# Performance work log

Measured on AMD Instinct MI355X. Metric: run time of the kernel, lower is better.

## Reference

```python
import jax, jax.numpy as jnp
import numpy as np

B, NV, L, NKG = 8, 100, 128, 923
NT = NV + 1 + NKG  # 1024 total nodes
DV, DK, DH, H, NLAYERS, VOCAB = 2048, 300, 1024, 8, 3, 50265
DHD = DH // H


def _ln(x, g, b, eps=1e-5):
    m = x.mean(-1, keepdims=True)
    v = x.var(-1, keepdims=True)
    return (x - m) / jnp.sqrt(v + eps) * g + b


def _gat_layer(x, mask, W, bb, a_src, a_dst, ln_g, ln_b):
    # x: [B,N,D], mask: [B,N,N] bool
    Bn, N, D = x.shape
    h = (x @ W + bb).reshape(Bn, N, H, DHD)
    s = jnp.einsum('bnhd,hd->bnh', h, a_src)  # source term
    t = jnp.einsum('bnhd,hd->bnh', h, a_dst)  # target term
    e = jax.nn.leaky_relu(s[:, :, None, :] + t[:, None, :, :], 0.2)  # [B,N,N,H]
    e = jnp.where(mask[..., None], e, -1e9)
    a = jax.nn.softmax(e, axis=2)  # over neighbors j
    out = jnp.einsum('bijh,bjhd->bihd', a, h).reshape(Bn, N, D)
    return _ln(x + out, ln_g, ln_b)


def setup_inputs() -> dict:
    key = jax.random.key(0)
    ks = jax.random.split(key, 24)
    s = 0.02
    inp = {
        'visual_features': jax.random.normal(ks[0], (B, NV, DV), jnp.float32),
        'question_input_ids': jax.random.randint(ks[1], (B, L), 0, VOCAB, jnp.int64) if False else jax.random.randint(ks[1], (B, L), 0, VOCAB).astype(jnp.int32),
        'question_attention_mask': jnp.ones((B, L), jnp.int32),
        'graph_node_features': jax.random.normal(ks[2], (B, NKG, DK), jnp.float32),
        'graph_adj': jax.random.randint(ks[3], (B, NT, NT), 0, 2).astype(jnp.int32),
        'graph_node_types': jax.random.randint(ks[4], (B, NT), 0, 3).astype(jnp.int32),
        # params
        'vis_W': jax.random.normal(ks[5], (DV, DH), jnp.float32) * s,
        'vis_b': jnp.zeros((DH,), jnp.float32),
        'vis_ln_g': jnp.ones((DH,), jnp.float32),
        'vis_ln_b': jnp.zeros((DH,), jnp.float32),
        'tok_emb': jax.random.normal(ks[6], (VOCAB, DH), jnp.float32) * s,
        'q_W': jax.random.normal(ks[7], (DH, DH), jnp.float32) * s,
        'q_b': jnp.zeros((DH,), jnp.float32),
        'q_ln_g': jnp.ones((DH,), jnp.float32),
        'q_ln_b': jnp.zeros((DH,), jnp.float32),
        'kg_W': jax.random.normal(ks[8], (DK, DH), jnp.float32) * s,
        'kg_b': jnp.zeros((DH,), jnp.float32),
        'kg_ln_g': jnp.ones((DH,), jnp.float32),
        'kg_ln_b': jnp.zeros((DH,), jnp.float32),
        'type_emb': jax.random.normal(ks[9], (3, DH), jnp.float32) * s,
        'gat_W': jax.random.normal(ks[10], (NLAYERS, DH, DH), jnp.float32) * s,
        'gat_b': jnp.zeros((NLAYERS, DH), jnp.float32),
        'a_src': jax.random.normal(ks[11], (NLAYERS, H, DHD), jnp.float32) * s,
        'a_dst': jax.random.normal(ks[12], (NLAYERS, H, DHD), jnp.float32) * s,
        'gat_ln_g': jnp.ones((NLAYERS, DH), jnp.float32),
        'gat_ln_b': jnp.zeros((NLAYERS, DH), jnp.float32),
        'readout_W': jax.random.normal(ks[13], (DH, 1), jnp.float32) * s,
        'readout_b': jnp.zeros((1,), jnp.float32),
        'cs_W1': jax.random.normal(ks[14], (DH, DH), jnp.float32) * s,
        'cs_b1': jnp.zeros((DH,), jnp.float32),
        'cs_W2': jax.random.normal(ks[15], (DH, 1), jnp.float32) * s,
        'cs_b2': jnp.zeros((1,), jnp.float32),
    }
    return inp


def reference(visual_features, question_input_ids, question_attention_mask,
              graph_node_features, graph_adj, graph_node_types,
              vis_W, vis_b, vis_ln_g, vis_ln_b,
              tok_emb, q_W, q_b, q_ln_g, q_ln_b,
              kg_W, kg_b, kg_ln_g, kg_ln_b,
              type_emb, gat_W, gat_b, a_src, a_dst, gat_ln_g, gat_ln_b,
              readout_W, readout_b, cs_W1, cs_b1, cs_W2, cs_b2):
    # 1. visual projection
    vis = _ln(visual_features @ vis_W + vis_b, vis_ln_g, vis_ln_b)  # [B,NV,DH]
    # 2. text encoder (embedding + masked mean-pool + proj + LN)
    te = tok_emb[question_input_ids]  # [B,L,DH]
    m = question_attention_mask.astype(te.dtype)[..., None]
    pooled = (te * m).sum(1) / jnp.maximum(m.sum(1), 1.0)
    q = _ln(pooled @ q_W + q_b, q_ln_g, q_ln_b)[:, None, :]  # [B,1,DH]
    # 3. KG projection
    kg = _ln(graph_node_features @ kg_W + kg_b, kg_ln_g, kg_ln_b)
    # 4-5. concat + node-type embeddings
    x = jnp.concatenate([vis, q, kg], axis=1) + type_emb[graph_node_types]
    # 6. dense GAT stack
    mask = graph_adj > 0
    for l in range(NLAYERS):
        x = _gat_layer(x, mask, gat_W[l], gat_b[l], a_src[l], a_dst[l],
                       gat_ln_g[l], gat_ln_b[l])
    # 7. attention-pooled readout
    w = jax.nn.softmax((x @ readout_W + readout_b).squeeze(-1), axis=-1)
    g = (x * w[..., None]).sum(1)  # [B,DH]
    # 8. candidate scorer
    logits = jax.nn.gelu(g @ cs_W1 + cs_b1) @ cs_W2 + cs_b2  # [B,1]
    return logits
```

## Files before the change

kernel.cpp:

```cpp
#include <hip/hip_runtime.h>
#include <math.h>

#define NB 8
#define NV 100
#define LQ 128
#define NKG 923
#define NT 1024
#define DV 2048
#define DK 300
#define DH 1024
#define NH 8
#define DHD 128
#define NLAYERS 3

typedef __attribute__((ext_vector_type(8))) short short8;
typedef __attribute__((ext_vector_type(4))) float f32x4;

__device__ __forceinline__ short f2bf(float f) {
    unsigned u = __float_as_uint(f);
    u += 0x7fff + ((u >> 16) & 1);
    return (short)(u >> 16);
}
__device__ __forceinline__ float bf2f(short s) {
    unsigned u = ((unsigned)(unsigned short)s) << 16;
    return __uint_as_float(u);
}
__device__ __forceinline__ unsigned pack2(float a, float b) {
    return (unsigned)(unsigned short)f2bf(a) | ((unsigned)(unsigned short)f2bf(b) << 16);
}

#if __has_builtin(__builtin_amdgcn_global_load_lds)
#define HAVE_GLL 1
__device__ __forceinline__ void gll16(const void* g, void* l) {
    __builtin_amdgcn_global_load_lds(
        (const __attribute__((address_space(1))) void*)g,
        (__attribute__((address_space(3))) void*)l, 16, 0, 0);
}
#else
#define HAVE_GLL 0
#endif

__device__ __forceinline__ float block_reduce_sum(float v, float* red) {
    int tid = threadIdx.x;
    red[tid] = v; __syncthreads();
    for (int s = 128; s > 0; s >>= 1) {
        if (tid < s) red[tid] += red[tid + s];
        __syncthreads();
    }
    float r = red[0]; __syncthreads();
    return r;
}
__device__ __forceinline__ float block_reduce_max(float v, float* red) {
    int tid = threadIdx.x;
    red[tid] = v; __syncthreads();
    for (int s = 128; s > 0; s >>= 1) {
        if (tid < s) red[tid] = fmaxf(red[tid], red[tid + s]);
        __syncthreads();
    }
    float r = red[0]; __syncthreads();
    return r;
}

__global__ __launch_bounds__(256) void bitmask_kernel(
    const int* __restrict__ adj, unsigned* __restrict__ mb)
{
    int bi = blockIdx.x;
    int tid = threadIdx.x;
#pragma unroll
    for (int p = 0; p < 4; ++p) {
        int j = p * 256 + tid;
        unsigned long long bal = __ballot(adj[(size_t)bi * NT + j] > 0);
        if ((tid & 63) == 0) {
            int w = (p * 256 + (tid & 0xC0)) >> 5;
            mb[(size_t)bi * 32 + w]     = (unsigned)bal;
            mb[(size_t)bi * 32 + w + 1] = (unsigned)(bal >> 32);
        }
    }
}

__global__ __launch_bounds__(256) void transpose_cast(
    const float* __restrict__ in, short* __restrict__ out,
    int K, int N, int Kp)
{
    __shared__ float ls[64][65];
    int n0 = blockIdx.x * 64, k0 = blockIdx.y * 64;
    int tid = threadIdx.x;
    int j4 = (tid & 15) * 4;
#pragma unroll
    for (int s = 0; s < 4; ++s) {
        int i = (tid >> 4) + s * 16;
        int k = k0 + i;
        float4 v = make_float4(0.f, 0.f, 0.f, 0.f);
        if (k < K) v = *(const float4*)(in + (size_t)k * N + n0 + j4);
        ls[i][j4 + 0] = v.x; ls[i][j4 + 1] = v.y;
        ls[i][j4 + 2] = v.z; ls[i][j4 + 3] = v.w;
    }
    __syncthreads();
#pragma unroll
    for (int s = 0; s < 4; ++s) {
        int a = (tid >> 4) + s * 16;
        int b = (tid & 15) * 4;
        uint2 pk;
        pk.x = pack2(ls[b + 0][a], ls[b + 1][a]);
        pk.y = pack2(ls[b + 2][a], ls[b + 3][a]);
        *(uint2*)(out + (size_t)(n0 + a) * Kp + k0 + b) = pk;
    }
}

__global__ __launch_bounds__(256) void gemm_bias_mfma(
    const float* __restrict__ A, const short* __restrict__ Wt,
    const float* __restrict__ bias, float* __restrict__ C,
    int M, int N, int K, int Kp, int ldA)
{
    __shared__ short At[128][32];
    __shared__ short Bt[128][32];
    int tid = threadIdx.x;
    int row0 = blockIdx.y * 128, col0 = blockIdx.x * 128;
    int lane = tid & 63, wave = tid >> 6;
    int quad = lane >> 4, lq = lane & 15;
    int wm = (wave >> 1) * 64, wn = (wave & 1) * 64;
    f32x4 acc[4][4];
#pragma unroll
    for (int i = 0; i < 4; ++i)
#pragma unroll
        for (int j = 0; j < 4; ++j) {
            f32x4 z = {0.f, 0.f, 0.f, 0.f};
            acc[i][j] = z;
        }
    int ar = tid >> 2;
    int ac = (tid & 3) * 8;
    for (int k0 = 0; k0 < Kp; k0 += 32) {
        bool fullk = (k0 + 32 <= K);
#pragma unroll
        for (int s = 0; s < 2; ++s) {
            int r = ar + s * 64;
            int grow = row0 + r;
            short8 pk;
            if (grow < M && fullk) {
                const float* src = A + (size_t)grow * ldA + k0 + ac;
                float4 v0 = *(const float4*)(src);
                float4 v1 = *(const float4*)(src + 4);
                pk[0] = f2bf(v0.x); pk[1] = f2bf(v0.y);
                pk[2] = f2bf(v0.z); pk[3] = f2bf(v0.w);
                pk[4] = f2bf(v1.x); pk[5] = f2bf(v1.y);
                pk[6] = f2bf(v1.z); pk[7] = f2bf(v1.w);
            } else {
#pragma unroll
                for (int e = 0; e < 8; ++e) {
                    int k = k0 + ac + e;
                    pk[e] = (grow < M && k < K)
                          ? f2bf(A[(size_t)grow * ldA + k]) : (short)0;
                }
            }
            *(short8*)&At[r][ac] = pk;
        }
#pragma unroll
        for (int s = 0; s < 2; ++s) {
            int n = ar + s * 64;
            short8 w = *(const short8*)(Wt + (size_t)(col0 + n) * Kp + k0 + ac);
            *(short8*)&Bt[n][ac] = w;
        }
        __syncthreads();
        short8 af[4], bfr[4];
#pragma unroll
        for (int i = 0; i < 4; ++i)
            af[i] = *(short8*)&At[wm + i * 16 + lq][quad * 8];
#pragma unroll
        for (int j = 0; j < 4; ++j)
            bfr[j] = *(short8*)&Bt[wn + j * 16 + lq][quad * 8];
#pragma unroll
        for (int i = 0; i < 4; ++i)
#pragma unroll
            for (int j = 0; j < 4; ++j)
                acc[i][j] = __builtin_amdgcn_mfma_f32_16x16x32_bf16(
                    af[i], bfr[j], acc[i][j], 0, 0, 0);
        __syncthreads();
    }
#pragma unroll
    for (int j = 0; j < 4; ++j) {
        int n = col0 + wn + j * 16 + lq;
        float bv = bias[n];
#pragma unroll
        for (int i = 0; i < 4; ++i) {
#pragma unroll
            for (int r = 0; r < 4; ++r) {
                int m = row0 + wm + i * 16 + quad * 4 + r;
                if (m < M) C[(size_t)m * N + n] = acc[i][j][r] + bv;
            }
        }
    }
}

__global__ __launch_bounds__(256) void gemm_st_mfma(
    const short* __restrict__ Ab,
    const short* __restrict__ Wt,
    const float* __restrict__ bias,
    const float* __restrict__ asrc,
    const float* __restrict__ adst,
    short* __restrict__ ht,
    float* __restrict__ sbuf, float* __restrict__ tbuf)
{
    __shared__ short At[128][32];
    __shared__ short Bt[128][32];
    __shared__ short ct[128][136];
    __shared__ float sred[2][128], tred[2][128];
    __shared__ float asl[128], adl[128];
    int tid = threadIdx.x;
    int h = blockIdx.x;
    int row0 = blockIdx.y * 128, col0 = h * 128;
    int b = row0 >> 10, i0 = row0 & 1023;
    int lane = tid & 63, wave = tid >> 6;
    int quad = lane >> 4, lq = lane & 15;
    int wm = (wave >> 1) * 64, wn = (wave & 1) * 64;
    if (tid < 128) asl[tid] = asrc[h * DHD + tid];
    else adl[tid - 128] = adst[h * DHD + tid - 128];
    f32x4 acc[4][4];
#pragma unroll
    for (int i = 0; i < 4; ++i)
#pragma unroll
        for (int j = 0; j < 4; ++j) {
            f32x4 z = {0.f, 0.f, 0.f, 0.f};
            acc[i][j] = z;
        }

    const short* gA0 = Ab + (size_t)(row0 + wave * 16 + (lane >> 2)) * DH + (lane & 3) * 8;
    const short* gA1 = gA0 + (size_t)64 * DH;
    const short* gB0 = Wt + (size_t)(col0 + wave * 16 + (lane >> 2)) * DH + (lane & 3) * 8;
    const short* gB1 = gB0 + (size_t)64 * DH;
#if HAVE_GLL
    char* lA0 = (char*)At + wave * 1024; char* lA1 = lA0 + 4096;
    char* lB0 = (char*)Bt + wave * 1024; char* lB1 = lB0 + 4096;
#endif
    for (int k0 = 0; k0 < DH; k0 += 32) {
#if HAVE_GLL
        gll16(gA0 + k0, lA0); gll16(gA1 + k0, lA1);
        gll16(gB0 + k0, lB0); gll16(gB1 + k0, lB1);
#else
        {
            short8 va0 = *(const short8*)(gA0 + k0);
            short8 va1 = *(const short8*)(gA1 + k0);
            short8 vb0 = *(const short8*)(gB0 + k0);
            short8 vb1 = *(const short8*)(gB1 + k0);
            *(short8*)((char*)At + wave * 1024 + lane * 16) = va0;
            *(short8*)((char*)At + 4096 + wave * 1024 + lane * 16) = va1;
            *(short8*)((char*)Bt + wave * 1024 + lane * 16) = vb0;
            *(short8*)((char*)Bt + 4096 + wave * 1024 + lane * 16) = vb1;
        }
#endif
        __syncthreads();
        short8 af[4], bfr[4];
#pragma unroll
        for (int i = 0; i < 4; ++i)
            af[i] = *(short8*)&At[wm + i * 16 + lq][quad * 8];
#pragma unroll
        for (int j = 0; j < 4; ++j)
            bfr[j] = *(short8*)&Bt[wn + j * 16 + lq][quad * 8];
#pragma unroll
        for (int i = 0; i < 4; ++i)
#pragma unroll
            for (int j = 0; j < 4; ++j)
                acc[i][j] = __builtin_amdgcn_mfma_f32_16x16x32_bf16(
                    af[i], bfr[j], acc[i][j], 0, 0, 0);
        __syncthreads();
    }
#pragma unroll
    for (int j = 0; j < 4; ++j) {
        int d = wn + j * 16 + lq;
        float bv = bias[col0 + d];
#pragma unroll
        for (int i2 = 0; i2 < 4; ++i2) {
            int m = wm + i2 * 16 + quad * 4;
            uint2 pk;
            pk.x = pack2(acc[i2][j][0] + bv, acc[i2][j][1] + bv);
            pk.y = pack2(acc[i2][j][2] + bv, acc[i2][j][3] + bv);
            *(uint2*)&ct[d][m] = pk;
        }
    }
    __syncthreads();
    {
        int d = tid >> 1, half = tid & 1;
        short* dst = ht + ((size_t)(b * NH + h) * DHD + d) * NT + i0 + half * 64;
        const short* src = &ct[d][half * 64];
#pragma unroll
        for (int q = 0; q < 8; ++q)
            *(short8*)(dst + q * 8) = *(const short8*)(src + q * 8);
    }
    {
        int i = tid >> 1, half = tid & 1;
        float sa = 0.f, ta = 0.f;
#pragma unroll 16
        for (int dd = 0; dd < 64; ++dd) {
            int d = half * 64 + dd;
            float hv = bf2f(ct[d][i]);
            sa += hv * asl[d];
            ta += hv * adl[d];
        }
        sred[half][i] = sa; tred[half][i] = ta;
    }
    __syncthreads();
    if (tid < 128) {
        size_t idx = (size_t)(b * NH + h) * NT + i0 + tid;
        sbuf[idx] = sred[0][tid] + sred[1][tid];
        tbuf[idx] = tred[0][tid] + tred[1][tid];
    }
}

__global__ __launch_bounds__(256) void ln_scatter(
    const float* __restrict__ src, float* __restrict__ x,
    const float* __restrict__ g, const float* __restrict__ bta,
    int rows, int npb, int node_off)
{
    __shared__ float red[256];
    int r = blockIdx.x;
    if (r >= rows) return;
    int tid = threadIdx.x;
    int b = r / npb, n = r % npb;
    float4 v = *(const float4*)(src + (size_t)r * DH + tid * 4);
    float s = v.x + v.y + v.z + v.w;
    float sq = v.x * v.x + v.y * v.y + v.z * v.z + v.w * v.w;
    float tot = block_reduce_sum(s, red);
    float totsq = block_reduce_sum(sq, red);
    float mean = tot * (1.0f / DH);
    float var = totsq * (1.0f / DH) - mean * mean;
    float rstd = 1.0f / sqrtf(var + 1e-5f);
    float4 gv = *(const float4*)(g + tid * 4);
    float4 bv = *(const float4*)(bta + tid * 4);
    float4 o;
    o.x = (v.x - mean) * rstd * gv.x + bv.x;
    o.y = (v.y - mean) * rstd * gv.y + bv.y;
    o.z = (v.z - mean) * rstd * gv.z + bv.z;
    o.w = (v.w - mean) * rstd * gv.w + bv.w;
    *(float4*)(x + ((size_t)(b * NT + node_off + n)) * DH + tid * 4) = o;
}

__global__ __launch_bounds__(256) void ln_residual(
    float* __restrict__ x, const float* __restrict__ o,
    const float* __restrict__ g, const float* __restrict__ bta,
    short* __restrict__ xb)
{
    __shared__ float red[256];
    int r = blockIdx.x;
    int tid = threadIdx.x;
    float* xr = x + (size_t)r * DH;
    float4 xv = *(float4*)(xr + tid * 4);
    float4 ov = *(const float4*)(o + (size_t)r * DH + tid * 4);
    float v0 = xv.x + ov.x, v1 = xv.y + ov.y, v2 = xv.z + ov.z, v3 = xv.w + ov.w;
    float s = v0 + v1 + v2 + v3;
    float sq = v0 * v0 + v1 * v1 + v2 * v2 + v3 * v3;
    float tot = block_reduce_sum(s, red);
    float totsq = block_reduce_sum(sq, red);
    float mean = tot * (1.0f / DH);
    float var = totsq * (1.0f / DH) - mean * mean;
    float rstd = 1.0f / sqrtf(var + 1e-5f);
    float4 gv = *(const float4*)(g + tid * 4);
    float4 bv = *(const float4*)(bta + tid * 4);
    float4 out;
    out.x = (v0 - mean) * rstd * gv.x + bv.x;
    out.y = (v1 - mean) * rstd * gv.y + bv.y;
    out.z = (v2 - mean) * rstd * gv.z + bv.z;
    out.w = (v3 - mean) * rstd * gv.w + bv.w;
    *(float4*)(xr + tid * 4) = out;
    uint2 pk;
    pk.x = pack2(out.x, out.y);
    pk.y = pack2(out.z, out.w);
    *(uint2*)(xb + (size_t)r * DH + tid * 4) = pk;
}

__global__ __launch_bounds__(256) void pool_kernel(
    const float* __restrict__ tok_emb, const int* __restrict__ ids,
    const int* __restrict__ amask, float* __restrict__ pooled)
{
    int b = blockIdx.x;
    int tid = threadIdx.x;
    float a0 = 0, a1 = 0, a2 = 0, a3 = 0;
    float denom = 0;
    for (int l = 0; l < LQ; ++l) {
        int id = ids[b * LQ + l];
        float m = (float)amask[b * LQ + l];
        denom += m;
        float4 e = *(const float4*)(tok_emb + (size_t)id * DH + tid * 4);
        a0 += m * e.x; a1 += m * e.y; a2 += m * e.z; a3 += m * e.w;
    }
    float inv = 1.0f / fmaxf(denom, 1.0f);
    float4 o = make_float4(a0 * inv, a1 * inv, a2 * inv, a3 * inv);
    *(float4*)(pooled + b * DH + tid * 4) = o;
}

__global__ __launch_bounds__(256) void type_add(
    float* __restrict__ x, const int* __restrict__ types,
    const float* __restrict__ type_emb, short* __restrict__ xb)
{
    int r = blockIdx.x;
    int tid = threadIdx.x;
    int ty = types[r];
    float4 xv = *(float4*)(x + (size_t)r * DH + tid * 4);
    float4 tv = *(const float4*)(type_emb + (size_t)ty * DH + tid * 4);
    xv.x += tv.x; xv.y += tv.y; xv.z += tv.z; xv.w += tv.w;
    *(float4*)(x + (size_t)r * DH + tid * 4) = xv;
    uint2 pk;
    pk.x = pack2(xv.x, xv.y);
    pk.y = pack2(xv.z, xv.w);
    *(uint2*)(xb + (size_t)r * DH + tid * 4) = pk;
}

__global__ __launch_bounds__(256) void stats_kernel(
    const unsigned* __restrict__ mb, const float* __restrict__ s,
    const float* __restrict__ t, float* __restrict__ mbuf, float* __restrict__ lbuf)
{
    __shared__ unsigned mwords[32];
    int bi = blockIdx.x;
    int b = bi >> 10, i = bi & 1023;
    int tid = threadIdx.x;
    int wave = tid >> 6, lane = tid & 63;
    if (tid < 32) mwords[tid] = mb[(size_t)bi * 32 + tid];
    __syncthreads();
#pragma unroll
    for (int hh = 0; hh < 2; ++hh) {
        int h = wave * 2 + hh;
        const float* tp = t + (size_t)(b * NH + h) * NT;
        float si = s[(size_t)(b * NH + h) * NT + i];
        float vals[16];
        float mx = -3e38f;
#pragma unroll
        for (int k = 0; k < 16; ++k) {
            int j = k * 64 + lane;
            float v = si + tp[j];
            v = v > 0.f ? v : 0.2f * v;
            bool on = (mwords[j >> 5] >> (j & 31)) & 1;
            v = on ? v : -1e9f;
            vals[k] = v;
            mx = fmaxf(mx, v);
        }
#pragma unroll
        for (int off = 32; off > 0; off >>= 1)
            mx = fmaxf(mx, __shfl_xor(mx, off, 64));
        float ls = 0.f;
#pragma unroll
        for (int k = 0; k < 16; ++k) ls += __expf(vals[k] - mx);
#pragma unroll
        for (int off = 32; off > 0; off >>= 1)
            ls += __shfl_xor(ls, off, 64);
        if (lane == 0) {
            mbuf[(size_t)(b * NH + h) * NT + i] = mx;
            lbuf[(size_t)(b * NH + h) * NT + i] = 1.0f / ls;
        }
    }
}

__global__ __launch_bounds__(256) void agg_mfma(
    const short* __restrict__ ht, const unsigned* __restrict__ mb,
    const float* __restrict__ s, const float* __restrict__ t,
    const float* __restrict__ mbuf, const float* __restrict__ lbuf,
    float* __restrict__ obuf)
{
    __shared__ short vt[128][72];
    __shared__ short at[64][72];
    __shared__ unsigned mrow[64][32];
    __shared__ float sv[64], mv[64], lv[64];
    int i0 = blockIdx.x * 64;
    int h = blockIdx.y, b = blockIdx.z;
    int tid = threadIdx.x;
    int lane = tid & 63, wave = tid >> 6;
    int quad = lane >> 4, lq = lane & 15;
    int wi = (wave >> 1) * 32;
    int wd = (wave & 1) * 64;
    if (tid < 64) {
        size_t idx = (size_t)(b * NH + h) * NT + i0 + tid;
        sv[tid] = s[idx]; mv[tid] = mbuf[idx]; lv[tid] = lbuf[idx];
    }
#pragma unroll
    for (int s2 = 0; s2 < 2; ++s2) {
        int f = tid + s2 * 256;
        int ii = f >> 3, w4 = (f & 7) * 4;
        *(uint4*)&mrow[ii][w4] =
            *(const uint4*)(mb + ((size_t)(b * NT + i0 + ii)) * 32 + w4);
    }
    const float* tptr = t + (size_t)(b * NH + h) * NT;
    const short* hbase = ht + ((size_t)(b * NH + h) * DHD) * NT;
    f32x4 acc[2][4];
#pragma unroll
    for (int i = 0; i < 2; ++i)
#pragma unroll
        for (int j = 0; j < 4; ++j) {
            f32x4 z = {0.f, 0.f, 0.f, 0.f};
            acc[i][j] = z;
        }
    int ii = tid >> 2;
    int jq = (tid & 3) * 16;
    for (int j0 = 0; j0 < NT; j0 += 64) {
        __syncthreads();
#pragma unroll
        for (int s2 = 0; s2 < 4; ++s2) {
            int f = tid + s2 * 256;
            int d = f >> 3, c = (f & 7) * 8;
            *(short8*)&vt[d][c] = *(const short8*)(hbase + (size_t)d * NT + j0 + c);
        }
        {
            unsigned mw = mrow[ii][(j0 + jq) >> 5] >> ((j0 + jq) & 31);
            float svv = sv[ii], mvv = mv[ii], lvv = lv[ii];
            float4 t0 = *(const float4*)(tptr + j0 + jq);
            float4 t1 = *(const float4*)(tptr + j0 + jq + 4);
            float4 t2 = *(const float4*)(tptr + j0 + jq + 8);
            float4 t3 = *(const float4*)(tptr + j0 + jq + 12);
            float tv16[16] = {t0.x, t0.y, t0.z, t0.w, t1.x, t1.y, t1.z, t1.w,
                              t2.x, t2.y, t2.z, t2.w, t3.x, t3.y, t3.z, t3.w};
            short8 p0, p1;
#pragma unroll
            for (int e = 0; e < 8; ++e) {
                float v = svv + tv16[e];
                v = v > 0.f ? v : 0.2f * v;
                float a = ((mw >> e) & 1) ? __expf(v - mvv) * lvv : 0.f;
                p0[e] = f2bf(a);
            }
#pragma unroll
            for (int e = 0; e < 8; ++e) {
                float v = svv + tv16[8 + e];
                v = v > 0.f ? v : 0.2f * v;
                float a = ((mw >> (8 + e)) & 1) ? __expf(v - mvv) * lvv : 0.f;
                p1[e] = f2bf(a);
            }
            *(short8*)&at[ii][jq] = p0;
            *(short8*)&at[ii][jq + 8] = p1;
        }
        __syncthreads();
#pragma unroll
        for (int ks = 0; ks < 2; ++ks) {
            short8 af[2], bfr[4];
            af[0] = *(short8*)&at[wi + lq][ks * 32 + quad * 8];
            af[1] = *(short8*)&at[wi + 16 + lq][ks * 32 + quad * 8];
#pragma unroll
            for (int j = 0; j < 4; ++j)
                bfr[j] = *(short8*)&vt[wd + j * 16 + lq][ks * 32 + quad * 8];
#pragma unroll
            for (int i2 = 0; i2 < 2; ++i2)
#pragma unroll
                for (int j = 0; j < 4; ++j)
                    acc[i2][j] = __builtin_amdgcn_mfma_f32_16x16x32_bf16(
                        af[i2], bfr[j], acc[i2][j], 0, 0, 0);
        }
    }
#pragma unroll
    for (int i2 = 0; i2 < 2; ++i2) {
#pragma unroll
        for (int r = 0; r < 4; ++r) {
            int i = i0 + wi + i2 * 16 + quad * 4 + r;
            float* dst = obuf + ((size_t)(b * NT + i)) * DH + h * DHD + wd;
#pragma unroll
            for (int j = 0; j < 4; ++j)
                dst[j * 16 + lq] = acc[i2][j][r];
        }
    }
}

__global__ __launch_bounds__(64) void score_kernel(
    const float* __restrict__ x, const float* __restrict__ rW,
    const float* __restrict__ rb, float* __restrict__ scores)
{
    int r = blockIdx.x;
    int lane = threadIdx.x;
    const float* xr = x + (size_t)r * DH;
    float acc = 0.f;
#pragma unroll
    for (int k = 0; k < 4; ++k) {
        float4 xv = *(const float4*)(xr + lane * 16 + k * 4);
        float4 wv = *(const float4*)(rW + lane * 16 + k * 4);
        acc += xv.x * wv.x + xv.y * wv.y + xv.z * wv.z + xv.w * wv.w;
    }
    for (int off = 32; off > 0; off >>= 1) acc += __shfl_down(acc, off, 64);
    if (lane == 0) scores[r] = acc + rb[0];
}

__global__ __launch_bounds__(256) void softmax_w(float* __restrict__ scores)
{
    __shared__ float red[256];
    int b = blockIdx.x;
    int tid = threadIdx.x;
    float* sr = scores + (size_t)b * NT;
    float v[4];
    float mx = -3e38f;
#pragma unroll
    for (int k = 0; k < 4; ++k) { v[k] = sr[tid + k * 256]; mx = fmaxf(mx, v[k]); }
    float m = block_reduce_max(mx, red);
    float ls = 0.f;
#pragma unroll
    for (int k = 0; k < 4; ++k) { v[k] = expf(v[k] - m); ls += v[k]; }
    float tot = block_reduce_sum(ls, red);
    float inv = 1.0f / tot;
#pragma unroll
    for (int k = 0; k < 4; ++k) sr[tid + k * 256] = v[k] * inv;
}

__global__ __launch_bounds__(256) void pool_part(
    const float* __restrict__ x, const float* __restrict__ w,
    float* __restrict__ gpart)
{
    int p = blockIdx.x;
    int b = blockIdx.y;
    int tid = threadIdx.x;
    float a0 = 0, a1 = 0, a2 = 0, a3 = 0;
    for (int n = p * 128; n < (p + 1) * 128; ++n) {
        float wv = w[(size_t)b * NT + n];
        float4 xv = *(const float4*)(x + ((size_t)(b * NT + n)) * DH + tid * 4);
        a0 += wv * xv.x; a1 += wv * xv.y; a2 += wv * xv.z; a3 += wv * xv.w;
    }
    float4 o = make_float4(a0, a1, a2, a3);
    *(float4*)(gpart + ((size_t)(b * 8 + p)) * DH + tid * 4) = o;
}

__global__ __launch_bounds__(256) void scorer_kernel(
    const float* __restrict__ gpart, const float* __restrict__ W1,
    const float* __restrict__ b1, const float* __restrict__ W2,
    const float* __restrict__ b2, float* __restrict__ out)
{
    __shared__ float gsh[DH];
    __shared__ float red[256];
    int b = blockIdx.x;
    int tid = threadIdx.x;
#pragma unroll
    for (int c = 0; c < 4; ++c) {
        int d = tid + c * 256;
        float gv = 0.f;
        for (int p = 0; p < 8; ++p) gv += gpart[((size_t)(b * 8 + p)) * DH + d];
        gsh[d] = gv;
    }
    __syncthreads();
    float acc[4] = {};
    for (int d = 0; d < DH; ++d) {
        float gv = gsh[d];
        const float* wr = W1 + (size_t)d * DH;
#pragma unroll
        for (int c = 0; c < 4; ++c) acc[c] += gv * wr[tid + c * 256];
    }
    float part = 0.f;
#pragma unroll
    for (int c = 0; c < 4; ++c) {
        int k = tid + c * 256;
        float u = acc[c] + b1[k];
        float inner = 0.7978845608028654f * (u + 0.044715f * u * u * u);
        float gel = 0.5f * u * (1.0f + tanhf(inner));
        part += gel * W2[k];
    }
    float tot = block_reduce_sum(part, red);
    if (tid == 0) out[b] = tot + b2[0];
}

extern "C" void kernel_launch(void* const* d_in, const int* in_sizes, int n_in,
                              void* d_out, int out_size, void* d_ws, size_t ws_size,
                              hipStream_t stream)
{
    const float* visual   = (const float*)d_in[0];
    const int*   q_ids    = (const int*)d_in[1];
    const int*   q_mask   = (const int*)d_in[2];
    const float* kg_feat  = (const float*)d_in[3];
    const int*   adj      = (const int*)d_in[4];
    const int*   ntypes   = (const int*)d_in[5];
    const float* vis_W    = (const float*)d_in[6];
    const float* vis_b    = (const float*)d_in[7];
    const float* vis_lng  = (const float*)d_in[8];
    const float* vis_lnb  = (const float*)d_in[9];
    const float* tok_emb  = (const float*)d_in[10];
    const float* q_W      = (const float*)d_in[11];
    const float* q_b      = (const float*)d_in[12];
    const float* q_lng    = (const float*)d_in[13];
    const float* q_lnb    = (const float*)d_in[14];
    const float* kg_W     = (const float*)d_in[15];
    const float* kg_b     = (const float*)d_in[16];
    const float* kg_lng   = (const float*)d_in[17];
    const float* kg_lnb   = (const float*)d_in[18];
    const float* type_emb = (const float*)d_in[19];
    const float* gat_W    = (const float*)d_in[20];
    const float* gat_b    = (const float*)d_in[21];
    const float* a_src    = (const float*)d_in[22];
    const float* a_dst    = (const float*)d_in[23];
    const float* gat_lng  = (const float*)d_in[24];
    const float* gat_lnb  = (const float*)d_in[25];
    const float* read_W   = (const float*)d_in[26];
    const float* read_b   = (const float*)d_in[27];
    const float* cs_W1    = (const float*)d_in[28];
    const float* cs_b1    = (const float*)d_in[29];
    const float* cs_W2    = (const float*)d_in[30];
    const float* cs_b2    = (const float*)d_in[31];
    float* out = (float*)d_out;

    float* ws = (float*)d_ws;
    const size_t NROW = (size_t)NB * NT;
    float* x      = ws;
    float* obuf   = x + NROW * DH;
    float* sbuf   = obuf + NROW * DH;
    float* tbuf   = sbuf + NB * NH * NT;
    float* mbuf   = tbuf + NB * NH * NT;
    float* lbuf   = mbuf + NB * NH * NT;
    float* pooled = lbuf + NB * NH * NT;
    float* scores = pooled + NB * DH;
    float* gpart  = scores + NROW;
    short* wt_gat = (short*)(gpart + NB * 8 * DH);
    short* ht     = wt_gat + (size_t)NLAYERS * DH * DH;
    unsigned* mb  = (unsigned*)(ht + (size_t)NB * NH * DHD * NT);
    short* xb     = (short*)(mb + (size_t)NB * NT * 32);
    short* wt_vis = xb + NROW * DH;
    short* wt_q   = wt_vis + (size_t)1024 * 2048;
    short* wt_kg  = wt_q + (size_t)1024 * 1024;

    transpose_cast<<<dim3(16, 32), 256, 0, stream>>>(vis_W, wt_vis, DV, DH, DV);
    transpose_cast<<<dim3(16, 16), 256, 0, stream>>>(q_W, wt_q, DH, DH, DH);
    transpose_cast<<<dim3(16, 5), 256, 0, stream>>>(kg_W, wt_kg, DK, DH, 320);
    for (int l = 0; l < NLAYERS; ++l)
        transpose_cast<<<dim3(16, 16), 256, 0, stream>>>(
            gat_W + (size_t)l * DH * DH, wt_gat + (size_t)l * DH * DH, DH, DH, DH);
    bitmask_kernel<<<NB * NT, 256, 0, stream>>>(adj, mb);

    gemm_bias_mfma<<<dim3(8, 7), 256, 0, stream>>>(
        visual, wt_vis, vis_b, obuf, NB * NV, DH, DV, DV, DV);
    ln_scatter<<<NB * NV, 256, 0, stream>>>(obuf, x, vis_lng, vis_lnb, NB * NV, NV, 0);

    pool_kernel<<<NB, 256, 0, stream>>>(tok_emb, q_ids, q_mask, pooled);
    gemm_bias_mfma<<<dim3(8, 1), 256, 0, stream>>>(
        pooled, wt_q, q_b, obuf, NB, DH, DH, DH, DH);
    ln_scatter<<<NB, 256, 0, stream>>>(obuf, x, q_lng, q_lnb, NB, 1, NV);

    gemm_bias_mfma<<<dim3(8, 58), 256, 0, stream>>>(
        kg_feat, wt_kg, kg_b, obuf, NB * NKG, DH, DK, 320, DK);
    ln_scatter<<<NB * NKG, 256, 0, stream>>>(obuf, x, kg_lng, kg_lnb, NB * NKG, NKG, NV + 1);

    type_add<<<NB * NT, 256, 0, stream>>>(x, ntypes, type_emb, xb);

    for (int l = 0; l < NLAYERS; ++l) {
        const float* bl  = gat_b + (size_t)l * DH;
        const float* asl = a_src + (size_t)l * NH * DHD;
        const float* adl = a_dst + (size_t)l * NH * DHD;
        gemm_st_mfma<<<dim3(NH, 64), 256, 0, stream>>>(
            xb, wt_gat + (size_t)l * DH * DH, bl, asl, adl, ht, sbuf, tbuf);
        stats_kernel<<<NB * NT, 256, 0, stream>>>(mb, sbuf, tbuf, mbuf, lbuf);
        agg_mfma<<<dim3(16, NH, NB), 256, 0, stream>>>(
            ht, mb, sbuf, tbuf, mbuf, lbuf, obuf);
        ln_residual<<<NB * NT, 256, 0, stream>>>(x, obuf,
            gat_lng + (size_t)l * DH, gat_lnb + (size_t)l * DH, xb);
    }

    score_kernel<<<NB * NT, 64, 0, stream>>>(x, read_W, read_b, scores);
    softmax_w<<<NB, 256, 0, stream>>>(scores);
    pool_part<<<dim3(8, NB), 256, 0, stream>>>(x, scores, gpart);
    scorer_kernel<<<NB, 256, 0, stream>>>(gpart, cs_W1, cs_b1, cs_W2, cs_b2, out);
}
```

Before: 1.096 ms.

## Fuse GAT softmax stats into aggregation with online softmax and fold readout kernels

The separate stats pass is removed; the aggregation kernel now computes the attention softmax online, keeping a running max and sum, rescaling the accumulators each tile and normalising once at the end. The readout score is folded into the last layer's LayerNorm-residual kernel, and the readout softmax moves into pool_part, dropping the score_kernel and softmax_w launches. gemm_st_mfma also reuses one LDS region for the A/B tiles and the output staging tile to cut shared-memory use. The intent is fewer launches and less global traffic for the max and sum buffers, at the cost of extra rescale work and exp evaluations inside the aggregation loop, plus redundant softmax reductions across the pool_part blocks.

```diff
diff --git a/kernel.cpp b/kernel.cpp
--- a/kernel.cpp
+++ b/kernel.cpp
@@ -192,17 +192,16 @@
 }
 
 __global__ __launch_bounds__(256) void gemm_st_mfma(
-    const short* __restrict__ Ab,
-    const short* __restrict__ Wt,
+    const short* __restrict__ Ab, const short* __restrict__ Wt,
     const float* __restrict__ bias,
-    const float* __restrict__ asrc,
-    const float* __restrict__ adst,
+    const float* __restrict__ asrc, const float* __restrict__ adst,
     short* __restrict__ ht,
     float* __restrict__ sbuf, float* __restrict__ tbuf)
 {
-    __shared__ short At[128][32];
-    __shared__ short Bt[128][32];
-    __shared__ short ct[128][136];
+    __shared__ __align__(16) short smem[17408];
+    short (*At)[32]  = (short(*)[32])smem;
+    short (*Bt)[32]  = (short(*)[32])(smem + 4096);
+    short (*ct)[136] = (short(*)[136])smem;
     __shared__ float sred[2][128], tred[2][128];
     __shared__ float asl[128], adl[128];
     int tid = threadIdx.x;
@@ -336,7 +335,9 @@
 __global__ __launch_bounds__(256) void ln_residual(
     float* __restrict__ x, const float* __restrict__ o,
     const float* __restrict__ g, const float* __restrict__ bta,
-    short* __restrict__ xb)
+    short* __restrict__ xb,
+    const float* __restrict__ rW, const float* __restrict__ rb,
+    float* __restrict__ scores)
 {
     __shared__ float red[256];
     int r = blockIdx.x;
@@ -364,6 +365,12 @@
     pk.x = pack2(out.x, out.y);
     pk.y = pack2(out.z, out.w);
     *(uint2*)(xb + (size_t)r * DH + tid * 4) = pk;
+    if (scores) {
+        float4 wv = *(const float4*)(rW + tid * 4);
+        float p = out.x * wv.x + out.y * wv.y + out.z * wv.z + out.w * wv.w;
+        float totp = block_reduce_sum(p, red);
+        if (tid == 0) scores[r] = totp + rb[0];
+    }
 }
 
 __global__ __launch_bounds__(256) void pool_kernel(
@@ -403,60 +410,15 @@
     *(uint2*)(xb + (size_t)r * DH + tid * 4) = pk;
 }
 
-__global__ __launch_bounds__(256) void stats_kernel(
-    const unsigned* __restrict__ mb, const float* __restrict__ s,
-    const float* __restrict__ t, float* __restrict__ mbuf, float* __restrict__ lbuf)
-{
-    __shared__ unsigned mwords[32];
-    int bi = blockIdx.x;
-    int b = bi >> 10, i = bi & 1023;
-    int tid = threadIdx.x;
-    int wave = tid >> 6, lane = tid & 63;
-    if (tid < 32) mwords[tid] = mb[(size_t)bi * 32 + tid];
-    __syncthreads();
-#pragma unroll
-    for (int hh = 0; hh < 2; ++hh) {
-        int h = wave * 2 + hh;
-        const float* tp = t + (size_t)(b * NH + h) * NT;
-        float si = s[(size_t)(b * NH + h) * NT + i];
-        float vals[16];
-        float mx = -3e38f;
-#pragma unroll
-        for (int k = 0; k < 16; ++k) {
-            int j = k * 64 + lane;
-            float v = si + tp[j];
-            v = v > 0.f ? v : 0.2f * v;
-            bool on = (mwords[j >> 5] >> (j & 31)) & 1;
-            v = on ? v : -1e9f;
-            vals[k] = v;
-            mx = fmaxf(mx, v);
-        }
-#pragma unroll
-        for (int off = 32; off > 0; off >>= 1)
-            mx = fmaxf(mx, __shfl_xor(mx, off, 64));
-        float ls = 0.f;
-#pragma unroll
-        for (int k = 0; k < 16; ++k) ls += __expf(vals[k] - mx);
-#pragma unroll
-        for (int off = 32; off > 0; off >>= 1)
-            ls += __shfl_xor(ls, off, 64);
-        if (lane == 0) {
-            mbuf[(size_t)(b * NH + h) * NT + i] = mx;
-            lbuf[(size_t)(b * NH + h) * NT + i] = 1.0f / ls;
-        }
-    }
-}
-
 __global__ __launch_bounds__(256) void agg_mfma(
     const short* __restrict__ ht, const unsigned* __restrict__ mb,
     const float* __restrict__ s, const float* __restrict__ t,
-    const float* __restrict__ mbuf, const float* __restrict__ lbuf,
     float* __restrict__ obuf)
 {
     __shared__ short vt[128][72];
     __shared__ short at[64][72];
     __shared__ unsigned mrow[64][32];
-    __shared__ float sv[64], mv[64], lv[64];
+    __shared__ float sv[64], alpha_s[64], lfin[64];
     int i0 = blockIdx.x * 64;
     int h = blockIdx.y, b = blockIdx.z;
     int tid = threadIdx.x;
@@ -464,16 +426,13 @@
     int quad = lane >> 4, lq = lane & 15;
     int wi = (wave >> 1) * 32;
     int wd = (wave & 1) * 64;
-    if (tid < 64) {
-        size_t idx = (size_t)(b * NH + h) * NT + i0 + tid;
-        sv[tid] = s[idx]; mv[tid] = mbuf[idx]; lv[tid] = lbuf[idx];
-    }
+    if (tid < 64) sv[tid] = s[(size_t)(b * NH + h) * NT + i0 + tid];
 #pragma unroll
     for (int s2 = 0; s2 < 2; ++s2) {
         int f = tid + s2 * 256;
-        int ii = f >> 3, w4 = (f & 7) * 4;
-        *(uint4*)&mrow[ii][w4] =
-            *(const uint4*)(mb + ((size_t)(b * NT + i0 + ii)) * 32 + w4);
+        int ii2 = f >> 3, w4 = (f & 7) * 4;
+        *(uint4*)&mrow[ii2][w4] =
+            *(const uint4*)(mb + ((size_t)(b * NT + i0 + ii2)) * 32 + w4);
     }
     const float* tptr = t + (size_t)(b * NH + h) * NT;
     const short* hbase = ht + ((size_t)(b * NH + h) * DHD) * NT;
@@ -487,6 +446,7 @@
         }
     int ii = tid >> 2;
     int jq = (tid & 3) * 16;
+    float m_run = -3e38f, l_run = 0.f;
     for (int j0 = 0; j0 < NT; j0 += 64) {
         __syncthreads();
 #pragma unroll
@@ -495,34 +455,59 @@
             int d = f >> 3, c = (f & 7) * 8;
             *(short8*)&vt[d][c] = *(const short8*)(hbase + (size_t)d * NT + j0 + c);
         }
+        float vv[16];
+        unsigned mw;
+        float tmax = -3e38f;
         {
-            unsigned mw = mrow[ii][(j0 + jq) >> 5] >> ((j0 + jq) & 31);
-            float svv = sv[ii], mvv = mv[ii], lvv = lv[ii];
+            mw = mrow[ii][(j0 + jq) >> 5] >> ((j0 + jq) & 31);
+            float svv = sv[ii];
             float4 t0 = *(const float4*)(tptr + j0 + jq);
             float4 t1 = *(const float4*)(tptr + j0 + jq + 4);
             float4 t2 = *(const float4*)(tptr + j0 + jq + 8);
             float4 t3 = *(const float4*)(tptr + j0 + jq + 12);
             float tv16[16] = {t0.x, t0.y, t0.z, t0.w, t1.x, t1.y, t1.z, t1.w,
                               t2.x, t2.y, t2.z, t2.w, t3.x, t3.y, t3.z, t3.w};
-            short8 p0, p1;
-#pragma unroll
-            for (int e = 0; e < 8; ++e) {
+#pragma unroll
+            for (int e = 0; e < 16; ++e) {
                 float v = svv + tv16[e];
                 v = v > 0.f ? v : 0.2f * v;
-                float a = ((mw >> e) & 1) ? __expf(v - mvv) * lvv : 0.f;
-                p0[e] = f2bf(a);
+                v = ((mw >> e) & 1) ? v : -1e9f;
+                vv[e] = v;
+                tmax = fmaxf(tmax, v);
             }
-#pragma unroll
-            for (int e = 0; e < 8; ++e) {
-                float v = svv + tv16[8 + e];
-                v = v > 0.f ? v : 0.2f * v;
-                float a = ((mw >> (8 + e)) & 1) ? __expf(v - mvv) * lvv : 0.f;
-                p1[e] = f2bf(a);
+        }
+        tmax = fmaxf(tmax, __shfl_xor(tmax, 1, 64));
+        tmax = fmaxf(tmax, __shfl_xor(tmax, 2, 64));
+        float m_new = fmaxf(m_run, tmax);
+        float al = __expf(m_run - m_new);
+        float tsum = 0.f;
+        short8 p0, p1;
+#pragma unroll
+        for (int e = 0; e < 8; ++e) {
+            float w = ((mw >> e) & 1) ? __expf(vv[e] - m_new) : 0.f;
+            tsum += w; p0[e] = f2bf(w);
+        }
+#pragma unroll
+        for (int e = 0; e < 8; ++e) {
+            float w = ((mw >> (8 + e)) & 1) ? __expf(vv[8 + e] - m_new) : 0.f;
+            tsum += w; p1[e] = f2bf(w);
+        }
+        tsum += __shfl_xor(tsum, 1, 64);
+        tsum += __shfl_xor(tsum, 2, 64);
+        l_run = l_run * al + tsum;
+        m_run = m_new;
+        *(short8*)&at[ii][jq] = p0;
+        *(short8*)&at[ii][jq + 8] = p1;
+        if ((tid & 3) == 0) alpha_s[ii] = al;
+        __syncthreads();
+#pragma unroll
+        for (int i2 = 0; i2 < 2; ++i2)
+#pragma unroll
+            for (int r = 0; r < 4; ++r) {
+                float arow = alpha_s[wi + i2 * 16 + quad * 4 + r];
+#pragma unroll
+                for (int j = 0; j < 4; ++j) acc[i2][j][r] *= arow;
             }
-            *(short8*)&at[ii][jq] = p0;
-            *(short8*)&at[ii][jq + 8] = p1;
-        }
-        __syncthreads();
 #pragma unroll
         for (int ks = 0; ks < 2; ++ks) {
             short8 af[2], bfr[4];
@@ -539,43 +524,31 @@
                         af[i2], bfr[j], acc[i2][j], 0, 0, 0);
         }
     }
+    if ((tid & 3) == 0) lfin[ii] = l_run;
+    __syncthreads();
 #pragma unroll
     for (int i2 = 0; i2 < 2; ++i2) {
 #pragma unroll
         for (int r = 0; r < 4; ++r) {
-            int i = i0 + wi + i2 * 16 + quad * 4 + r;
-            float* dst = obuf + ((size_t)(b * NT + i)) * DH + h * DHD + wd;
+            int il = wi + i2 * 16 + quad * 4 + r;
+            float inv = 1.0f / lfin[il];
+            float* dst = obuf + ((size_t)(b * NT + i0 + il)) * DH + h * DHD + wd;
 #pragma unroll
             for (int j = 0; j < 4; ++j)
-                dst[j * 16 + lq] = acc[i2][j][r];
-        }
-    }
-}
-
-__global__ __launch_bounds__(64) void score_kernel(
-    const float* __restrict__ x, const float* __restrict__ rW,
-    const float* __restrict__ rb, float* __restrict__ scores)
-{
-    int r = blockIdx.x;
-    int lane = threadIdx.x;
-    const float* xr = x + (size_t)r * DH;
-    float acc = 0.f;
-#pragma unroll
-    for (int k = 0; k < 4; ++k) {
-        float4 xv = *(const float4*)(xr + lane * 16 + k * 4);
-        float4 wv = *(const float4*)(rW + lane * 16 + k * 4);
-        acc += xv.x * wv.x + xv.y * wv.y + xv.z * wv.z + xv.w * wv.w;
-    }
-    for (int off = 32; off > 0; off >>= 1) acc += __shfl_down(acc, off, 64);
-    if (lane == 0) scores[r] = acc + rb[0];
-}
-
-__global__ __launch_bounds__(256) void softmax_w(float* __restrict__ scores)
+                dst[j * 16 + lq] = acc[i2][j][r] * inv;
+        }
+    }
+}
+
+__global__ __launch_bounds__(256) void pool_part(
+    const float* __restrict__ x, const float* __restrict__ scores,
+    float* __restrict__ gpart)
 {
     __shared__ float red[256];
-    int b = blockIdx.x;
-    int tid = threadIdx.x;
-    float* sr = scores + (size_t)b * NT;
+    int p = blockIdx.x;
+    int b = blockIdx.y;
+    int tid = threadIdx.x;
+    const float* sr = scores + (size_t)b * NT;
     float v[4];
     float mx = -3e38f;
 #pragma unroll
@@ -583,23 +556,12 @@
     float m = block_reduce_max(mx, red);
     float ls = 0.f;
 #pragma unroll
-    for (int k = 0; k < 4; ++k) { v[k] = expf(v[k] - m); ls += v[k]; }
+    for (int k = 0; k < 4; ++k) ls += expf(v[k] - m);
     float tot = block_reduce_sum(ls, red);
     float inv = 1.0f / tot;
-#pragma unroll
-    for (int k = 0; k < 4; ++k) sr[tid + k * 256] = v[k] * inv;
-}
-
-__global__ __launch_bounds__(256) void pool_part(
-    const float* __restrict__ x, const float* __restrict__ w,
-    float* __restrict__ gpart)
-{
-    int p = blockIdx.x;
-    int b = blockIdx.y;
-    int tid = threadIdx.x;
     float a0 = 0, a1 = 0, a2 = 0, a3 = 0;
     for (int n = p * 128; n < (p + 1) * 128; ++n) {
-        float wv = w[(size_t)b * NT + n];
+        float wv = expf(sr[n] - m) * inv;
         float4 xv = *(const float4*)(x + ((size_t)(b * NT + n)) * DH + tid * 4);
         a0 += wv * xv.x; a1 += wv * xv.y; a2 += wv * xv.z; a3 += wv * xv.w;
     }
@@ -688,9 +650,7 @@
     float* obuf   = x + NROW * DH;
     float* sbuf   = obuf + NROW * DH;
     float* tbuf   = sbuf + NB * NH * NT;
-    float* mbuf   = tbuf + NB * NH * NT;
-    float* lbuf   = mbuf + NB * NH * NT;
-    float* pooled = lbuf + NB * NH * NT;
+    float* pooled = tbuf + NB * NH * NT;
     float* scores = pooled + NB * DH;
     float* gpart  = scores + NROW;
     short* wt_gat = (short*)(gpart + NB * 8 * DH);
@@ -730,15 +690,13 @@
         const float* adl = a_dst + (size_t)l * NH * DHD;
         gemm_st_mfma<<<dim3(NH, 64), 256, 0, stream>>>(
             xb, wt_gat + (size_t)l * DH * DH, bl, asl, adl, ht, sbuf, tbuf);
-        stats_kernel<<<NB * NT, 256, 0, stream>>>(mb, sbuf, tbuf, mbuf, lbuf);
         agg_mfma<<<dim3(16, NH, NB), 256, 0, stream>>>(
-            ht, mb, sbuf, tbuf, mbuf, lbuf, obuf);
+            ht, mb, sbuf, tbuf, obuf);
         ln_residual<<<NB * NT, 256, 0, stream>>>(x, obuf,
-            gat_lng + (size_t)l * DH, gat_lnb + (size_t)l * DH, xb);
-    }
-
-    score_kernel<<<NB * NT, 64, 0, stream>>>(x, read_W, read_b, scores);
-    softmax_w<<<NB, 256, 0, stream>>>(scores);
+            gat_lng + (size_t)l * DH, gat_lnb + (size_t)l * DH, xb,
+            read_W, read_b, (l == NLAYERS - 1) ? scores : nullptr);
+    }
+
     pool_part<<<dim3(8, NB), 256, 0, stream>>>(x, scores, gpart);
     scorer_kernel<<<NB, 256, 0, stream>>>(gpart, cs_W1, cs_b1, cs_W2, cs_b2, out);
 }
```

New measurement: 1.059 ms. 3.4% less time.
